# Kernel optimization log

Measured on AMD Instinct MI355X. Metric: run time of the kernel, lower is better.

The kernel has to match this reference:

```python
import jax, jax.numpy as jnp
import numpy as np

CLAMP_MIN = 0.001
DOWN = 4  # ROI module downsampling factor


def setup_inputs() -> dict:
    key = jax.random.key(0)
    ks = jax.random.split(key, 12)
    B, I, H, W = 2, 63, 320, 320
    C, HID, CTX = 14, 128, 192
    h4, w4 = H // DOWN, W // DOWN
    return {
        "depth": jnp.zeros((B, 1, H, W), jnp.float32),
        "context": jax.random.normal(ks[0], (B, CTX, h4, w4), jnp.float32),
        "input_feature_map": jax.random.normal(ks[1], (B, HID, h4, w4), jnp.float32),
        "bin_num": 16,
        "min_depth": 1,
        "max_depth": 10,
        "masks": jnp.zeros((B, 1, H, W), jnp.float32),
        "instances": jax.random.randint(ks[2], (B, I, H, W), 0, 2).astype(jnp.int32),
        "boxes": jax.random.randint(ks[3], (B, I, 4), 0, W).astype(jnp.int32),
        "labels": jax.random.randint(ks[4], (B, I), 0, C).astype(jnp.int32),
        # per-class scale/shift heads (row 0 = invalid class, gathered but masked out)
        "W_scale": (jax.random.normal(ks[5], (C, HID), jnp.float32) * 0.05),
        "b_scale": (jax.random.normal(ks[6], (C,), jnp.float32) * 0.05),
        "W_shift": (jax.random.normal(ks[7], (C, HID), jnp.float32) * 0.05),
        "b_shift": (jax.random.normal(ks[8], (C,), jnp.float32) * 0.05),
        # shared canonical head: 1x1 conv 128 -> 1
        "Wc": (jax.random.normal(ks[9], (HID,), jnp.float32) * 0.05),
        "bc": (jax.random.normal(ks[10], (), jnp.float32) * 0.05),
    }


def reference(depth, context, input_feature_map, bin_num, min_depth, max_depth,
              masks, instances, boxes, labels,
              W_scale, b_scale, W_shift, b_shift, Wc, bc):
    B, I, H, W = instances.shape
    m = instances.astype(input_feature_map.dtype)            # [B,I,H,W] binary instance masks
    m_ds = m[:, :, ::DOWN, ::DOWN]                            # [B,I,H/4,W/4] mask at feature res
    valid = (labels != 0).astype(input_feature_map.dtype)     # [B,I]

    # Per-instance mask-pooled feature (vectorized gather over all instances/classes)
    denom = jnp.maximum(m_ds.sum(axis=(-1, -2)), 1.0)         # [B,I]
    pooled = jnp.einsum('bihw,bchw->bic', m_ds, input_feature_map) / denom[..., None]  # [B,I,HID]

    # Per-class scale/shift heads, gathered by label; zero where label==0
    scale = (jnp.einsum('bic,bic->bi', pooled, W_scale[labels]) + b_scale[labels]) * valid  # [B,I]
    shift = (jnp.einsum('bic,bic->bi', pooled, W_shift[labels]) + b_shift[labels]) * valid  # [B,I]

    # invalid instances stay zero (mirrors zero-init scatter of canonical_full)
    can_small = jnp.einsum('bchw,c->bhw', input_feature_map, Wc) + bc   # [B,H/4,W/4]
    can = jnp.repeat(jnp.repeat(can_small, DOWN, axis=-2), DOWN, axis=-1)  # [B,H,W]
    canonical_full = can[:, None] * m * valid[..., None, None]          # [B,I,H,W]

    # loss_type == 0 path: relu then clamp(min=0.001)
    depth_instances_r = jnp.maximum(
        jax.nn.relu(canonical_full * scale[..., None, None] + shift[..., None, None]),
        CLAMP_MIN)

    return depth_instances_r, canonical_full, scale, shift
```

## Files before the change

kernel.cpp:

```cpp
#include <hip/hip_runtime.h>

#define NB 2
#define NI 63
#define BI (NB*NI)
#define HW 320
#define HWF (HW*HW)
#define H4 80
#define HW4 (H4*H4)
#define HID 128
#define IFM_B (HID*HW4)

#define OUT_DEPTH 0
#define OUT_CAN   (BI*HWF)
#define OUT_SCALE (2*BI*HWF)
#define OUT_SHIFT (2*BI*HWF + BI)

#define KB 64
#define NKB (HW4/KB)
#define FPAD 68
#define PROW 132
#define PBLK (64*PROW)

typedef int   vint4  __attribute__((ext_vector_type(4)));
typedef float vflt4  __attribute__((ext_vector_type(4)));

__global__ __launch_bounds__(512) void pool_gemm_kernel(
    const int* __restrict__ inst, const float* __restrict__ ifm,
    const float* __restrict__ Wc, const float* __restrict__ bc,
    float* __restrict__ can_ws, float* __restrict__ partial) {
  __shared__ float fT[128][FPAD];
  __shared__ float mT[64][FPAD];
  __shared__ float wc_s[128];

  int bid = blockIdx.x;
  int b = bid / NKB, kb = bid % NKB;
  int k0 = kb * KB;
  int t = threadIdx.x;

  if (t < 128) wc_s[t] = Wc[t];

  const float* fbase = ifm + (long)b * IFM_B;
#pragma unroll
  for (int s = 0; s < 4; ++s) {
    int v = s * 512 + t;
    int c = v >> 4;
    int jq = v & 15;
    float4 x = *(const float4*)(fbase + c * HW4 + k0 + jq * 4);
    *(float4*)&fT[c][jq * 4] = x;
  }
#pragma unroll
  for (int s = 0; s < 8; ++s) {
    int v = s * 512 + t;
    int i = v >> 6;
    int j = v & 63;
    int hw4 = k0 + j;
    int r = hw4 / H4, col = hw4 - r * H4;
    float m = 0.f;
    if (i < NI)
      m = (float)__builtin_nontemporal_load(
          inst + ((long)(b * NI + i)) * HWF + r * 4 * HW + col * 4);
    mT[i][j] = m;
  }
  __syncthreads();

  int ti = t >> 5, tc = t & 31;
  int i0 = ti * 4;
  float acc[4][4];
#pragma unroll
  for (int u = 0; u < 4; ++u)
#pragma unroll
    for (int v = 0; v < 4; ++v) acc[u][v] = 0.f;

  for (int k = 0; k < KB; k += 4) {
    float4 a[4], bb[4];
#pragma unroll
    for (int u = 0; u < 4; ++u) a[u] = *(const float4*)&mT[i0 + u][k];
#pragma unroll
    for (int v = 0; v < 4; ++v) bb[v] = *(const float4*)&fT[tc + 32 * v][k];
#pragma unroll
    for (int u = 0; u < 4; ++u)
#pragma unroll
      for (int v = 0; v < 4; ++v)
        acc[u][v] += a[u].x * bb[v].x + a[u].y * bb[v].y +
                     a[u].z * bb[v].z + a[u].w * bb[v].w;
  }

  float* pb = partial + (long)bid * PBLK;
#pragma unroll
  for (int u = 0; u < 4; ++u)
#pragma unroll
    for (int v = 0; v < 4; ++v)
      pb[(i0 + u) * PROW + tc + 32 * v] = acc[u][v];

  if (t < 64) {
    float ms = 0.f;
#pragma unroll
    for (int q = 0; q < KB / 4; ++q) {
      float4 m4 = *(const float4*)&mT[t][q * 4];
      ms += m4.x + m4.y + m4.z + m4.w;
    }
    pb[t * PROW + 128] = ms;

    float ca = bc[0];
#pragma unroll 8
    for (int c = 0; c < 128; ++c) ca += fT[c][t] * wc_s[c];
    can_ws[b * HW4 + k0 + t] = ca;
  }
}

__global__ __launch_bounds__(512) void finish_kernel(
    const float* __restrict__ partial, const int* __restrict__ labels,
    const float* __restrict__ W_scale, const float* __restrict__ b_scale,
    const float* __restrict__ W_shift, const float* __restrict__ b_shift,
    float* __restrict__ scale_out, float* __restrict__ shift_out) {
  __shared__ float pooled4[4][128];

  int bi = blockIdx.x;
  int b = bi / NI, i = bi % NI;
  int t = threadIdx.x;
  int g = t >> 7;
  int c = t & 127;

  const float* pb = partial + ((long)b * NKB) * PBLK + i * PROW;

  float acc = 0.f;
#pragma unroll
  for (int q = 0; q < 25; ++q)
    acc += __builtin_nontemporal_load(&pb[(long)(g * 25 + q) * PBLK + c]);
  pooled4[g][c] = acc;
  __syncthreads();

  if (t < 64) {
    float ms = pb[(long)t * PBLK + 128];
    if (t + 64 < NKB) ms += pb[(long)(t + 64) * PBLK + 128];
    for (int off = 32; off; off >>= 1) ms += __shfl_down(ms, off, 64);
    ms = __shfl(ms, 0, 64);

    int lab = labels[bi];
    float valid = (lab != 0) ? 1.f : 0.f;
    float inv = 1.f / fmaxf(ms, 1.f);
    float p0 = pooled4[0][t] + pooled4[1][t] + pooled4[2][t] + pooled4[3][t];
    float p1 = pooled4[0][t + 64] + pooled4[1][t + 64] +
               pooled4[2][t + 64] + pooled4[3][t + 64];
    const float* ws = W_scale + lab * HID;
    const float* wh = W_shift + lab * HID;
    float sa = p0 * ws[t] + p1 * ws[t + 64];
    float sh = p0 * wh[t] + p1 * wh[t + 64];
    for (int off = 32; off; off >>= 1) {
      sa += __shfl_down(sa, off, 64);
      sh += __shfl_down(sh, off, 64);
    }
    if (t == 0) {
      scale_out[bi] = (sa * inv + b_scale[lab]) * valid;
      shift_out[bi] = (sh * inv + b_shift[lab]) * valid;
    }
  }
}

__global__ __launch_bounds__(256) void out_kernel(
    const int* __restrict__ inst, const float* __restrict__ can_ws,
    const int* __restrict__ labels,
    const float* __restrict__ scale_arr, const float* __restrict__ shift_arr,
    float* __restrict__ out_depth, float* __restrict__ out_can) {
  int blk = blockIdx.x;
  int bi = blk / 50;
  int chunk = blk - bi * 50;
  int b = bi / NI;
  int pix = chunk * 2048 + threadIdx.x * 8;
  int h = pix / HW, w = pix - h * HW;

  const float2 c2 = *(const float2*)(can_ws + b * HW4 + (h >> 2) * H4 + (w >> 2));
  int lab = labels[bi];
  float valid = (lab != 0) ? 1.f : 0.f;
  float sc = scale_arr[bi];
  float sh = shift_arr[bi];
  float cv0 = c2.x * valid;
  float cv1 = c2.y * valid;

  long base = (long)bi * HWF + pix;
  const vint4 iv0 = __builtin_nontemporal_load((const vint4*)(inst + base));
  const vint4 iv1 = __builtin_nontemporal_load((const vint4*)(inst + base + 4));
  vflt4 cf0, cf1, df0, df1;
  cf0.x = cv0 * (float)iv0.x;
  cf0.y = cv0 * (float)iv0.y;
  cf0.z = cv0 * (float)iv0.z;
  cf0.w = cv0 * (float)iv0.w;
  cf1.x = cv1 * (float)iv1.x;
  cf1.y = cv1 * (float)iv1.y;
  cf1.z = cv1 * (float)iv1.z;
  cf1.w = cv1 * (float)iv1.w;
  df0.x = fmaxf(cf0.x * sc + sh, 0.001f);
  df0.y = fmaxf(cf0.y * sc + sh, 0.001f);
  df0.z = fmaxf(cf0.z * sc + sh, 0.001f);
  df0.w = fmaxf(cf0.w * sc + sh, 0.001f);
  df1.x = fmaxf(cf1.x * sc + sh, 0.001f);
  df1.y = fmaxf(cf1.y * sc + sh, 0.001f);
  df1.z = fmaxf(cf1.z * sc + sh, 0.001f);
  df1.w = fmaxf(cf1.w * sc + sh, 0.001f);
  __builtin_nontemporal_store(cf0, (vflt4*)(out_can + base));
  __builtin_nontemporal_store(cf1, (vflt4*)(out_can + base + 4));
  __builtin_nontemporal_store(df0, (vflt4*)(out_depth + base));
  __builtin_nontemporal_store(df1, (vflt4*)(out_depth + base + 4));
}

extern "C" void kernel_launch(void* const* d_in, const int* in_sizes, int n_in,
                              void* d_out, int out_size, void* d_ws, size_t ws_size,
                              hipStream_t stream) {
  const float* ifm     = (const float*)d_in[2];
  const int*   inst    = (const int*)d_in[7];
  const int*   labels  = (const int*)d_in[9];
  const float* W_scale = (const float*)d_in[10];
  const float* b_scale = (const float*)d_in[11];
  const float* W_shift = (const float*)d_in[12];
  const float* b_shift = (const float*)d_in[13];
  const float* Wc      = (const float*)d_in[14];
  const float* bc      = (const float*)d_in[15];

  float* out       = (float*)d_out;
  float* out_depth = out + OUT_DEPTH;
  float* out_can   = out + OUT_CAN;
  float* out_scale = out + OUT_SCALE;
  float* out_shift = out + OUT_SHIFT;

  float* can_ws  = (float*)d_ws;
  float* partial = (float*)d_ws + 2 * HW4;

  pool_gemm_kernel<<<NB * NKB, 512, 0, stream>>>(inst, ifm, Wc, bc,
                                                 can_ws, partial);
  finish_kernel<<<BI, 512, 0, stream>>>(partial, labels, W_scale, b_scale,
                                        W_shift, b_shift, out_scale, out_shift);
  out_kernel<<<BI * 50, 256, 0, stream>>>(inst, can_ws, labels, out_scale,
                                          out_shift, out_depth, out_can);
}
```

Before: 201.3 us.

## Fuse three kernels into one persistent kernel with grid barriers

```diff
diff --git a/kernel.cpp b/kernel.cpp
--- a/kernel.cpp
+++ b/kernel.cpp
@@ -17,190 +17,216 @@
 
 #define KB 64
 #define NKB (HW4/KB)
+#define NPOOL (NB*NKB)
 #define FPAD 68
 #define PROW 132
 #define PBLK (64*PROW)
 
+#define GRID 256
+#define VBPX 4096
+#define NVB (BI*(HWF/VBPX))
+
 typedef int   vint4  __attribute__((ext_vector_type(4)));
 typedef float vflt4  __attribute__((ext_vector_type(4)));
 
-__global__ __launch_bounds__(512) void pool_gemm_kernel(
+__device__ __forceinline__ void grid_barrier(unsigned* ctr) {
+  __syncthreads();
+  if (threadIdx.x == 0) {
+    __threadfence();
+    unsigned old = atomicAdd(ctr, 1u);
+    if (old == GRID - 1) {
+      __hip_atomic_store(ctr, 0u, __ATOMIC_RELEASE, __HIP_MEMORY_SCOPE_AGENT);
+    } else {
+      while (__hip_atomic_load(ctr, __ATOMIC_ACQUIRE,
+                               __HIP_MEMORY_SCOPE_AGENT) != 0u)
+        __builtin_amdgcn_s_sleep(2);
+    }
+    __threadfence();
+  }
+  __syncthreads();
+}
+
+__global__ __launch_bounds__(512) void fused_kernel(
     const int* __restrict__ inst, const float* __restrict__ ifm,
     const float* __restrict__ Wc, const float* __restrict__ bc,
-    float* __restrict__ can_ws, float* __restrict__ partial) {
-  __shared__ float fT[128][FPAD];
-  __shared__ float mT[64][FPAD];
-  __shared__ float wc_s[128];
-
-  int bid = blockIdx.x;
-  int b = bid / NKB, kb = bid % NKB;
-  int k0 = kb * KB;
-  int t = threadIdx.x;
-
-  if (t < 128) wc_s[t] = Wc[t];
-
-  const float* fbase = ifm + (long)b * IFM_B;
-#pragma unroll
-  for (int s = 0; s < 4; ++s) {
-    int v = s * 512 + t;
-    int c = v >> 4;
-    int jq = v & 15;
-    float4 x = *(const float4*)(fbase + c * HW4 + k0 + jq * 4);
-    *(float4*)&fT[c][jq * 4] = x;
-  }
-#pragma unroll
-  for (int s = 0; s < 8; ++s) {
-    int v = s * 512 + t;
-    int i = v >> 6;
-    int j = v & 63;
-    int hw4 = k0 + j;
-    int r = hw4 / H4, col = hw4 - r * H4;
-    float m = 0.f;
-    if (i < NI)
-      m = (float)__builtin_nontemporal_load(
-          inst + ((long)(b * NI + i)) * HWF + r * 4 * HW + col * 4);
-    mT[i][j] = m;
-  }
-  __syncthreads();
-
-  int ti = t >> 5, tc = t & 31;
-  int i0 = ti * 4;
-  float acc[4][4];
-#pragma unroll
-  for (int u = 0; u < 4; ++u)
-#pragma unroll
-    for (int v = 0; v < 4; ++v) acc[u][v] = 0.f;
-
-  for (int k = 0; k < KB; k += 4) {
-    float4 a[4], bb[4];
-#pragma unroll
-    for (int u = 0; u < 4; ++u) a[u] = *(const float4*)&mT[i0 + u][k];
-#pragma unroll
-    for (int v = 0; v < 4; ++v) bb[v] = *(const float4*)&fT[tc + 32 * v][k];
-#pragma unroll
-    for (int u = 0; u < 4; ++u)
-#pragma unroll
-      for (int v = 0; v < 4; ++v)
-        acc[u][v] += a[u].x * bb[v].x + a[u].y * bb[v].y +
-                     a[u].z * bb[v].z + a[u].w * bb[v].w;
-  }
-
-  float* pb = partial + (long)bid * PBLK;
-#pragma unroll
-  for (int u = 0; u < 4; ++u)
-#pragma unroll
-    for (int v = 0; v < 4; ++v)
-      pb[(i0 + u) * PROW + tc + 32 * v] = acc[u][v];
-
-  if (t < 64) {
-    float ms = 0.f;
-#pragma unroll
-    for (int q = 0; q < KB / 4; ++q) {
-      float4 m4 = *(const float4*)&mT[t][q * 4];
-      ms += m4.x + m4.y + m4.z + m4.w;
-    }
-    pb[t * PROW + 128] = ms;
-
-    float ca = bc[0];
-#pragma unroll 8
-    for (int c = 0; c < 128; ++c) ca += fT[c][t] * wc_s[c];
-    can_ws[b * HW4 + k0 + t] = ca;
-  }
-}
-
-__global__ __launch_bounds__(512) void finish_kernel(
-    const float* __restrict__ partial, const int* __restrict__ labels,
+    const int* __restrict__ labels,
     const float* __restrict__ W_scale, const float* __restrict__ b_scale,
     const float* __restrict__ W_shift, const float* __restrict__ b_shift,
+    float* __restrict__ can_ws, float* __restrict__ partial,
+    unsigned* __restrict__ bars,
+    float* __restrict__ out_depth, float* __restrict__ out_can,
     float* __restrict__ scale_out, float* __restrict__ shift_out) {
-  __shared__ float pooled4[4][128];
-
-  int bi = blockIdx.x;
-  int b = bi / NI, i = bi % NI;
+  __shared__ union {
+    struct { float fT[128][FPAD]; float mT[64][FPAD]; float wc_s[128]; } p;
+    struct { float pooled4[4][128]; } f;
+  } sm;
+
+  int bid = blockIdx.x;
   int t = threadIdx.x;
-  int g = t >> 7;
-  int c = t & 127;
-
-  const float* pb = partial + ((long)b * NKB) * PBLK + i * PROW;
-
-  float acc = 0.f;
-#pragma unroll
-  for (int q = 0; q < 25; ++q)
-    acc += __builtin_nontemporal_load(&pb[(long)(g * 25 + q) * PBLK + c]);
-  pooled4[g][c] = acc;
-  __syncthreads();
-
-  if (t < 64) {
-    float ms = pb[(long)t * PBLK + 128];
-    if (t + 64 < NKB) ms += pb[(long)(t + 64) * PBLK + 128];
-    for (int off = 32; off; off >>= 1) ms += __shfl_down(ms, off, 64);
-    ms = __shfl(ms, 0, 64);
-
+
+  if (bid < NPOOL) {
+    int b = bid / NKB, kb = bid % NKB;
+    int k0 = kb * KB;
+
+    if (t < 128) sm.p.wc_s[t] = Wc[t];
+
+    const float* fbase = ifm + (long)b * IFM_B;
+#pragma unroll
+    for (int s = 0; s < 4; ++s) {
+      int v = s * 512 + t;
+      int c = v >> 4;
+      int jq = v & 15;
+      float4 x = *(const float4*)(fbase + c * HW4 + k0 + jq * 4);
+      *(float4*)&sm.p.fT[c][jq * 4] = x;
+    }
+#pragma unroll
+    for (int s = 0; s < 8; ++s) {
+      int v = s * 512 + t;
+      int i = v >> 6;
+      int j = v & 63;
+      int hw4 = k0 + j;
+      int r = hw4 / H4, col = hw4 - r * H4;
+      float m = 0.f;
+      if (i < NI)
+        m = (float)__builtin_nontemporal_load(
+            inst + ((long)(b * NI + i)) * HWF + r * 4 * HW + col * 4);
+      sm.p.mT[i][j] = m;
+    }
+    __syncthreads();
+
+    int ti = t >> 5, tc = t & 31;
+    int i0 = ti * 4;
+    float acc[4][4];
+#pragma unroll
+    for (int u = 0; u < 4; ++u)
+#pragma unroll
+      for (int v = 0; v < 4; ++v) acc[u][v] = 0.f;
+
+    for (int k = 0; k < KB; k += 4) {
+      float4 a[4], bb[4];
+#pragma unroll
+      for (int u = 0; u < 4; ++u) a[u] = *(const float4*)&sm.p.mT[i0 + u][k];
+#pragma unroll
+      for (int v = 0; v < 4; ++v) bb[v] = *(const float4*)&sm.p.fT[tc + 32 * v][k];
+#pragma unroll
+      for (int u = 0; u < 4; ++u)
+#pragma unroll
+        for (int v = 0; v < 4; ++v)
+          acc[u][v] += a[u].x * bb[v].x + a[u].y * bb[v].y +
+                       a[u].z * bb[v].z + a[u].w * bb[v].w;
+    }
+
+    float* pb = partial + (long)bid * PBLK;
+#pragma unroll
+    for (int u = 0; u < 4; ++u)
+#pragma unroll
+      for (int v = 0; v < 4; ++v)
+        pb[(i0 + u) * PROW + tc + 32 * v] = acc[u][v];
+
+    if (t < 64) {
+      float ms = 0.f;
+#pragma unroll
+      for (int q = 0; q < KB / 4; ++q) {
+        float4 m4 = *(const float4*)&sm.p.mT[t][q * 4];
+        ms += m4.x + m4.y + m4.z + m4.w;
+      }
+      pb[t * PROW + 128] = ms;
+
+      float ca = bc[0];
+#pragma unroll 8
+      for (int c = 0; c < 128; ++c) ca += sm.p.fT[c][t] * sm.p.wc_s[c];
+      can_ws[b * HW4 + k0 + t] = ca;
+    }
+  }
+
+  grid_barrier(&bars[0]);
+
+  if (bid < BI) {
+    int bi = bid;
+    int b = bi / NI, i = bi % NI;
+    int g = t >> 7;
+    int c = t & 127;
+
+    const float* pb = partial + ((long)b * NKB) * PBLK + i * PROW;
+
+    float acc = 0.f;
+#pragma unroll
+    for (int q = 0; q < 25; ++q)
+      acc += __builtin_nontemporal_load(&pb[(long)(g * 25 + q) * PBLK + c]);
+    sm.f.pooled4[g][c] = acc;
+    __syncthreads();
+
+    if (t < 64) {
+      float ms = pb[(long)t * PBLK + 128];
+      if (t + 64 < NKB) ms += pb[(long)(t + 64) * PBLK + 128];
+      for (int off = 32; off; off >>= 1) ms += __shfl_down(ms, off, 64);
+      ms = __shfl(ms, 0, 64);
+
+      int lab = labels[bi];
+      float valid = (lab != 0) ? 1.f : 0.f;
+      float inv = 1.f / fmaxf(ms, 1.f);
+      float p0 = sm.f.pooled4[0][t] + sm.f.pooled4[1][t] +
+                 sm.f.pooled4[2][t] + sm.f.pooled4[3][t];
+      float p1 = sm.f.pooled4[0][t + 64] + sm.f.pooled4[1][t + 64] +
+                 sm.f.pooled4[2][t + 64] + sm.f.pooled4[3][t + 64];
+      const float* ws = W_scale + lab * HID;
+      const float* wh = W_shift + lab * HID;
+      float sa = p0 * ws[t] + p1 * ws[t + 64];
+      float sh = p0 * wh[t] + p1 * wh[t + 64];
+      for (int off = 32; off; off >>= 1) {
+        sa += __shfl_down(sa, off, 64);
+        sh += __shfl_down(sh, off, 64);
+      }
+      if (t == 0) {
+        scale_out[bi] = (sa * inv + b_scale[lab]) * valid;
+        shift_out[bi] = (sh * inv + b_shift[lab]) * valid;
+      }
+    }
+  }
+
+  grid_barrier(&bars[1]);
+
+  for (int vb = bid; vb < NVB; vb += GRID) {
+    int bi = vb / (HWF / VBPX);
+    int chunk = vb - bi * (HWF / VBPX);
+    int b = bi / NI;
+    int pix = chunk * VBPX + t * 8;
+    int h = pix / HW, w = pix - h * HW;
+
+    const float2 c2 =
+        *(const float2*)(can_ws + b * HW4 + (h >> 2) * H4 + (w >> 2));
     int lab = labels[bi];
     float valid = (lab != 0) ? 1.f : 0.f;
-    float inv = 1.f / fmaxf(ms, 1.f);
-    float p0 = pooled4[0][t] + pooled4[1][t] + pooled4[2][t] + pooled4[3][t];
-    float p1 = pooled4[0][t + 64] + pooled4[1][t + 64] +
-               pooled4[2][t + 64] + pooled4[3][t + 64];
-    const float* ws = W_scale + lab * HID;
-    const float* wh = W_shift + lab * HID;
-    float sa = p0 * ws[t] + p1 * ws[t + 64];
-    float sh = p0 * wh[t] + p1 * wh[t + 64];
-    for (int off = 32; off; off >>= 1) {
-      sa += __shfl_down(sa, off, 64);
-      sh += __shfl_down(sh, off, 64);
-    }
-    if (t == 0) {
-      scale_out[bi] = (sa * inv + b_scale[lab]) * valid;
-      shift_out[bi] = (sh * inv + b_shift[lab]) * valid;
-    }
-  }
-}
-
-__global__ __launch_bounds__(256) void out_kernel(
-    const int* __restrict__ inst, const float* __restrict__ can_ws,
-    const int* __restrict__ labels,
-    const float* __restrict__ scale_arr, const float* __restrict__ shift_arr,
-    float* __restrict__ out_depth, float* __restrict__ out_can) {
-  int blk = blockIdx.x;
-  int bi = blk / 50;
-  int chunk = blk - bi * 50;
-  int b = bi / NI;
-  int pix = chunk * 2048 + threadIdx.x * 8;
-  int h = pix / HW, w = pix - h * HW;
-
-  const float2 c2 = *(const float2*)(can_ws + b * HW4 + (h >> 2) * H4 + (w >> 2));
-  int lab = labels[bi];
-  float valid = (lab != 0) ? 1.f : 0.f;
-  float sc = scale_arr[bi];
-  float sh = shift_arr[bi];
-  float cv0 = c2.x * valid;
-  float cv1 = c2.y * valid;
-
-  long base = (long)bi * HWF + pix;
-  const vint4 iv0 = __builtin_nontemporal_load((const vint4*)(inst + base));
-  const vint4 iv1 = __builtin_nontemporal_load((const vint4*)(inst + base + 4));
-  vflt4 cf0, cf1, df0, df1;
-  cf0.x = cv0 * (float)iv0.x;
-  cf0.y = cv0 * (float)iv0.y;
-  cf0.z = cv0 * (float)iv0.z;
-  cf0.w = cv0 * (float)iv0.w;
-  cf1.x = cv1 * (float)iv1.x;
-  cf1.y = cv1 * (float)iv1.y;
-  cf1.z = cv1 * (float)iv1.z;
-  cf1.w = cv1 * (float)iv1.w;
-  df0.x = fmaxf(cf0.x * sc + sh, 0.001f);
-  df0.y = fmaxf(cf0.y * sc + sh, 0.001f);
-  df0.z = fmaxf(cf0.z * sc + sh, 0.001f);
-  df0.w = fmaxf(cf0.w * sc + sh, 0.001f);
-  df1.x = fmaxf(cf1.x * sc + sh, 0.001f);
-  df1.y = fmaxf(cf1.y * sc + sh, 0.001f);
-  df1.z = fmaxf(cf1.z * sc + sh, 0.001f);
-  df1.w = fmaxf(cf1.w * sc + sh, 0.001f);
-  __builtin_nontemporal_store(cf0, (vflt4*)(out_can + base));
-  __builtin_nontemporal_store(cf1, (vflt4*)(out_can + base + 4));
-  __builtin_nontemporal_store(df0, (vflt4*)(out_depth + base));
-  __builtin_nontemporal_store(df1, (vflt4*)(out_depth + base + 4));
+    float sc = scale_out[bi];
+    float sh = shift_out[bi];
+    float cv0 = c2.x * valid;
+    float cv1 = c2.y * valid;
+
+    long base = (long)bi * HWF + pix;
+    const vint4 iv0 = __builtin_nontemporal_load((const vint4*)(inst + base));
+    const vint4 iv1 = __builtin_nontemporal_load((const vint4*)(inst + base + 4));
+    vflt4 cf0, cf1, df0, df1;
+    cf0.x = cv0 * (float)iv0.x;
+    cf0.y = cv0 * (float)iv0.y;
+    cf0.z = cv0 * (float)iv0.z;
+    cf0.w = cv0 * (float)iv0.w;
+    cf1.x = cv1 * (float)iv1.x;
+    cf1.y = cv1 * (float)iv1.y;
+    cf1.z = cv1 * (float)iv1.z;
+    cf1.w = cv1 * (float)iv1.w;
+    df0.x = fmaxf(cf0.x * sc + sh, 0.001f);
+    df0.y = fmaxf(cf0.y * sc + sh, 0.001f);
+    df0.z = fmaxf(cf0.z * sc + sh, 0.001f);
+    df0.w = fmaxf(cf0.w * sc + sh, 0.001f);
+    df1.x = fmaxf(cf1.x * sc + sh, 0.001f);
+    df1.y = fmaxf(cf1.y * sc + sh, 0.001f);
+    df1.z = fmaxf(cf1.z * sc + sh, 0.001f);
+    df1.w = fmaxf(cf1.w * sc + sh, 0.001f);
+    __builtin_nontemporal_store(cf0, (vflt4*)(out_can + base));
+    __builtin_nontemporal_store(cf1, (vflt4*)(out_can + base + 4));
+    __builtin_nontemporal_store(df0, (vflt4*)(out_depth + base));
+    __builtin_nontemporal_store(df1, (vflt4*)(out_depth + base + 4));
+  }
 }
 
 extern "C" void kernel_launch(void* const* d_in, const int* in_sizes, int n_in,
@@ -222,13 +248,12 @@
   float* out_scale = out + OUT_SCALE;
   float* out_shift = out + OUT_SHIFT;
 
-  float* can_ws  = (float*)d_ws;
-  float* partial = (float*)d_ws + 2 * HW4;
-
-  pool_gemm_kernel<<<NB * NKB, 512, 0, stream>>>(inst, ifm, Wc, bc,
-                                                 can_ws, partial);
-  finish_kernel<<<BI, 512, 0, stream>>>(partial, labels, W_scale, b_scale,
-                                        W_shift, b_shift, out_scale, out_shift);
-  out_kernel<<<BI * 50, 256, 0, stream>>>(inst, can_ws, labels, out_scale,
-                                          out_shift, out_depth, out_can);
+  unsigned* bars  = (unsigned*)d_ws;
+  float* can_ws   = (float*)d_ws + 16;
+  float* partial  = can_ws + 2 * HW4;
+
+  hipMemsetAsync(bars, 0, 2 * sizeof(unsigned), stream);
+  fused_kernel<<<GRID, 512, 0, stream>>>(
+      inst, ifm, Wc, bc, labels, W_scale, b_scale, W_shift, b_shift,
+      can_ws, partial, bars, out_depth, out_can, out_scale, out_shift);
 }
```

After: 264.9 us. 31.5% more time.
